# Optimization experiments

Hardware: AMD Instinct MI355X
Metric: run time of the kernel (lower is better)

## Reference

```python
import jax, jax.numpy as jnp
import numpy as np

TEMPERATURE = 0.5


def setup_inputs() -> dict:
    key = jax.random.key(0)
    ks = jax.random.split(key, 12)
    B, N, T = 128, 64, 256
    IN, H, OUT = N + T, 256, 128
    E = N * (N - 1) // 2  # 2016 upper-tri edges per graph
    total_edges = B * E
    inp = {
        "x_topology": jax.random.normal(ks[0], (B, N, N), jnp.float32),
        "x_temporal": jax.random.normal(ks[1], (B, N, T), jnp.float32),
        "gumbel_u": jax.random.uniform(ks[2], (total_edges,), jnp.float32, 1e-6, 1.0),
        # GNNLayer linear
        "W_gnn": jax.random.normal(ks[3], (IN, H), jnp.float32) / np.sqrt(IN),
        "b_gnn": jnp.zeros((H,), jnp.float32),
        # edge heads (input dim 2*H)
        "W_mean": jax.random.normal(ks[4], (2 * H, OUT), jnp.float32) / np.sqrt(2 * H),
        "b_mean": jnp.zeros((OUT,), jnp.float32),
        "W_var": jax.random.normal(ks[5], (2 * H, OUT), jnp.float32) / np.sqrt(2 * H),
        "b_var": jnp.zeros((OUT,), jnp.float32),
        "W_w": jax.random.normal(ks[6], (2 * H, 1), jnp.float32) / np.sqrt(2 * H),
        "b_w": jnp.zeros((1,), jnp.float32),
    }
    return inp


def reference(x_topology, x_temporal, gumbel_u, W_gnn, b_gnn,
              W_mean, b_mean, W_var, b_var, W_w, b_w):
    B, N, _ = x_topology.shape
    T = x_temporal.shape[-1]
    # Upper-triangular fully-connected edge index (no self loops), batched with node offsets.
    row, col = jnp.triu_indices(N, k=1)          # [E]
    E = row.shape[0]
    offs = (jnp.arange(B) * N)[:, None]          # [B,1]
    src = (row[None, :] + offs).reshape(-1)       # [B*E]
    dst = (col[None, :] + offs).reshape(-1)       # [B*E]

    # Node features: concat topology + temporal, flatten batch of graphs.
    x = jnp.concatenate([x_topology, x_temporal], axis=-1).reshape(B * N, N + T)

    # Mean aggregation (PyG aggr='mean'): messages x[src] scattered to dst; 0 for isolated nodes.
    msg_sum = jax.ops.segment_sum(x[src], dst, num_segments=B * N)      # [B*N, N+T]
    cnt = jax.ops.segment_sum(jnp.ones_like(src, x.dtype), dst, num_segments=B * N)
    agg = jnp.where(cnt[:, None] > 0, msg_sum / jnp.maximum(cnt, 1.0)[:, None], 0.0)

    h = jax.nn.relu(agg @ W_gnn + b_gnn)          # [B*N, H]

    # Edge MLP heads on gathered [src||dst] embeddings.
    ef = jnp.concatenate([h[src], h[dst]], axis=-1)        # [B*E, 2H]
    mean = ef @ W_mean + b_mean                             # [B*E, OUT]
    variance = jax.nn.softplus(ef @ W_var + b_var) + 1e-6   # [B*E, OUT]
    weight = jax.nn.sigmoid((ef @ W_w + b_w)[:, 0])          # [B*E]

    # Gumbel-softmax over the flattened edge-weight vector (dim=-1 of a 1-D tensor).
    g = -jnp.log(-jnp.log(gumbel_u))
    gumbel_w = jax.nn.softmax((weight + g) / TEMPERATURE, axis=-1)

    # Gaussian similarity per edge, scatter into dense adjacency.
    sim = jnp.exp(-0.5 * jnp.mean(mean ** 2 / (variance + 1e-8), axis=-1))
    edge_w = sim * gumbel_w                                  # [B*E]

    b_idx = jnp.repeat(jnp.arange(B), E)
    adj = jnp.zeros((B, N, N), x.dtype).at[b_idx, jnp.tile(row, B), jnp.tile(col, B)].set(edge_w)
    return adj
```

## Files before the change

kernel.cpp:

```cpp
#include <hip/hip_runtime.h>
#include <hip/hip_bf16.h>
#include <math.h>

#define Bg   128
#define Nn   64
#define Tt   256
#define INF  320
#define Hd   256
#define OUTD 128
#define Ee   2016
#define TOTE (Bg*Ee)
#define SCOLS 576
#define MROWS 8192

typedef __attribute__((ext_vector_type(8))) short bf16x8;
typedef __attribute__((ext_vector_type(4))) float f32x4;

static __device__ __forceinline__ ushort f2bf(float v) {
    __hip_bfloat16 h = __float2bfloat16(v);
    return *(ushort*)&h;
}

#define CVT_N (INF * Hd)
#define PACK_N (Hd * SCOLS)
#define AGG_BLKS (Bg * 5)

__global__ __launch_bounds__(256) void k_agg_prep(
        const float* __restrict__ topo, const float* __restrict__ temp,
        const float* __restrict__ Wg, const float* __restrict__ Wm,
        const float* __restrict__ Wv, const float* __restrict__ Ww,
        const float* __restrict__ bm, const float* __restrict__ bv,
        const float* __restrict__ bw,
        ushort* __restrict__ agg, ushort* __restrict__ WgbS,
        ushort* __restrict__ WcatS, float* __restrict__ ebias,
        unsigned* __restrict__ red) {
    __shared__ float T[64 * 65];
    const int bid = blockIdx.x;
    const int tid = threadIdx.x;

    if (bid < AGG_BLKS) {
        const int b = bid / 5, ft = bid - 5 * (bid / 5);
        const int row = tid >> 2, seg = tid & 3;
        const float* src = (ft == 0) ? (topo + (size_t)(b * Nn + row) * Nn)
                                     : (temp + (size_t)(b * Nn + row) * Tt + (ft - 1) * 64);
        #pragma unroll
        for (int i = 0; i < 4; ++i) {
            float4 v = *(const float4*)(src + seg * 16 + i * 4);
            float* d = &T[row * 65 + seg * 16 + i * 4];
            d[0] = v.x; d[1] = v.y; d[2] = v.z; d[3] = v.w;
        }
        __syncthreads();
        const int w = tid >> 6, lane = tid & 63;
        #pragma unroll
        for (int k = 0; k < 16; ++k) {
            int f = w * 16 + k;
            float x = T[lane * 65 + f];
            float incl = x;
            #pragma unroll
            for (int o = 1; o < 64; o <<= 1) {
                float t = __shfl_up(incl, o);
                if (lane >= o) incl += t;
            }
            float excl = incl - x;
            T[lane * 65 + f] = lane ? excl * __builtin_amdgcn_rcpf((float)lane) : 0.f;
        }
        __syncthreads();
        const int node = tid >> 2, f0 = (tid & 3) * 16;
        ushort tmp[16];
        #pragma unroll
        for (int i = 0; i < 16; ++i) tmp[i] = f2bf(T[node * 65 + f0 + i]);
        ushort* dst = agg + (size_t)(b * Nn + node) * INF + ft * 64 + f0;
        *(uint4*)dst = *(uint4*)tmp;
        *(uint4*)(dst + 8) = *(uint4*)(tmp + 8);
        return;
    }

    int idx = (bid - AGG_BLKS) * 256 + tid;
    if (idx == 0) { red[0] = 0u; red[1] = 0u; }
    if (idx < CVT_N) {
        int j = idx & 7, lane = (idx >> 3) & 63, ns = (idx >> 9) & 3;
        int rem = idx >> 11;
        int kw = rem % 10, t = rem / 10;
        int n = t * 64 + ns * 16 + (lane & 15);
        int k = kw * 32 + (lane >> 4) * 8 + j;
        WgbS[idx] = f2bf(Wg[k * Hd + n]);
        return;
    }
    idx -= CVT_N;
    if (idx < PACK_N) {
        int j = idx & 7, lane = (idx >> 3) & 63, ns = (idx >> 9) & 3;
        int rem = idx >> 11;
        int kw = rem % 8, t = rem / 8;
        int n = t * 64 + ns * 16 + (lane & 15);
        int k = kw * 32 + (lane >> 4) * 8 + j;
        float v = 0.f;
        if (n < 128)       v = Wm[k * 128 + n];
        else if (n < 256)  v = Wm[(256 + k) * 128 + (n - 128)];
        else if (n < 384)  v = Wv[k * 128 + (n - 256)];
        else if (n < 512)  v = Wv[(256 + k) * 128 + (n - 384)];
        else if (n == 512) v = Ww[k];
        else if (n == 513) v = Ww[256 + k];
        WcatS[idx] = f2bf(v);
        return;
    }
    idx -= PACK_N;
    if (idx >= SCOLS) return;
    float e = 0.f;
    if (idx < 128)                    e = bm[idx];
    else if (idx >= 256 && idx < 384) e = bv[idx - 256];
    else if (idx == 512)              e = bw[0];
    ebias[idx] = e;
}

template<int K>
__global__ __launch_bounds__(256) void k_gemm_direct(const ushort* __restrict__ A,
                                                     const ushort* __restrict__ Bsw,
                                                     const float* __restrict__ bias,
                                                     ushort* __restrict__ Cb,
                                                     float* __restrict__ Cf,
                                                     int N, int relu, int transC) {
    const int tid = threadIdx.x;
    const int w = tid >> 6, lane = tid & 63;
    const int quad = lane >> 4, r16 = lane & 15;
    const int m0 = blockIdx.y * 64, n0 = blockIdx.x * 64;
    const ushort* arow = A + (size_t)(m0 + w * 16 + r16) * K + quad * 8;
    const ushort* bbase = Bsw + (size_t)blockIdx.x * (K / 32) * 2048 + lane * 8;
    f32x4 acc[4] = {};

    #pragma unroll 2
    for (int kw = 0; kw < K / 32; ++kw) {
        bf16x8 af = *(const bf16x8*)(arow + kw * 32);
        const ushort* bp = bbase + kw * 2048;
        bf16x8 b0 = *(const bf16x8*)(bp);
        bf16x8 b1 = *(const bf16x8*)(bp + 512);
        bf16x8 b2 = *(const bf16x8*)(bp + 1024);
        bf16x8 b3 = *(const bf16x8*)(bp + 1536);
        acc[0] = __builtin_amdgcn_mfma_f32_16x16x32_bf16(af, b0, acc[0], 0, 0, 0);
        acc[1] = __builtin_amdgcn_mfma_f32_16x16x32_bf16(af, b1, acc[1], 0, 0, 0);
        acc[2] = __builtin_amdgcn_mfma_f32_16x16x32_bf16(af, b2, acc[2], 0, 0, 0);
        acc[3] = __builtin_amdgcn_mfma_f32_16x16x32_bf16(af, b3, acc[3], 0, 0, 0);
    }

    const int row0 = m0 + w * 16 + quad * 4;
    #pragma unroll
    for (int ns = 0; ns < 4; ++ns) {
        f32x4 a = acc[ns];
        int col = n0 + ns * 16 + r16;
        float bb = bias ? bias[col] : 0.f;
        float vv[4];
        #pragma unroll
        for (int i = 0; i < 4; ++i) {
            float v = a[i] + bb;
            if (relu) v = fmaxf(v, 0.f);
            vv[i] = v;
        }
        if (transC) {
            *(float4*)(Cf + (size_t)col * MROWS + row0) = make_float4(vv[0], vv[1], vv[2], vv[3]);
        } else {
            #pragma unroll
            for (int i = 0; i < 4; ++i) {
                int row2 = row0 + i;
                if (Cb) Cb[(size_t)row2 * N + col] = f2bf(vv[i]);
                else    Cf[(size_t)row2 * N + col] = vv[i];
            }
        }
    }
}

static __device__ __forceinline__ float eterm(float pm, float qm, float pv, float qv) {
    float m = pm + qm;
    float x = pv + qv;
    float sp = fmaxf(x, 0.f) + __logf(1.f + __expf(-fabsf(x)));
    return m * m * __builtin_amdgcn_rcpf(sp + 1.01e-6f);
}

__global__ __launch_bounds__(256) void k_edge4(const float* __restrict__ ST,
                                               const float* __restrict__ gu,
                                               float* __restrict__ numer,
                                               unsigned* __restrict__ red) {
    __shared__ float L[4][16][132];
    __shared__ float sm[256];
    const int p = blockIdx.x % 10, b = blockIdx.x / 10;
    const int G0v[10] = {0,0,0,0,1,1,1,2,2,3};
    const int G1v[10] = {0,1,2,3,1,2,3,2,3,3};
    const int g0 = G0v[p], g1 = G1v[p];
    const int tid = threadIdx.x;

    #pragma unroll
    for (int rep = 0; rep < 8; ++rep) {
        int it = tid + 256 * rep;
        int arr = it >> 9;
        int c = (it >> 2) & 127, nq = it & 3;
        int g = (arr & 1) ? g1 : g0;
        float4 v = *(const float4*)&ST[(size_t)(arr * 128 + c) * MROWS + b * 64 + g * 16 + nq * 4];
        L[arr][nq * 4 + 0][c] = v.x;
        L[arr][nq * 4 + 1][c] = v.y;
        L[arr][nq * 4 + 2][c] = v.z;
        L[arr][nq * 4 + 3][c] = v.w;
    }
    __syncthreads();

    const int i = tid >> 4, j = tid & 15;
    float acc = 0.f;
    #pragma unroll 4
    for (int t = 0; t < 128; t += 4) {
        float4 mi = *(const float4*)&L[0][i][t];
        float4 mj = *(const float4*)&L[1][j][t];
        float4 vi = *(const float4*)&L[2][i][t];
        float4 vj = *(const float4*)&L[3][j][t];
        acc += eterm(mi.x, mj.x, vi.x, vj.x);
        acc += eterm(mi.y, mj.y, vi.y, vj.y);
        acc += eterm(mi.z, mj.z, vi.z, vj.z);
        acc += eterm(mi.w, mj.w, vi.w, vj.w);
    }

    const int ni = g0 * 16 + i, nj = g1 * 16 + j;
    float en = 0.f;
    if (ni < nj) {
        int e = b * Ee + (ni * (127 - ni)) / 2 + (nj - ni - 1);
        float se = __expf(acc * (-1.f / 256.f));
        float wr = ST[(size_t)512 * MROWS + b * 64 + ni]
                 + ST[(size_t)513 * MROWS + b * 64 + nj];
        float w  = __builtin_amdgcn_rcpf(1.f + __expf(-wr));
        float g  = -__logf(-__logf(gu[e]));
        en = __expf((w + g) * 2.0f);
        numer[e] = se * en;
    }
    sm[tid] = en; __syncthreads();
    for (int s = 128; s; s >>= 1) {
        if (tid < s) sm[tid] += sm[tid + s];
        __syncthreads();
    }
    if (!tid) atomicAdd((float*)&red[1], sm[0]);
}

__global__ void k_out(const float* __restrict__ numer, const unsigned* __restrict__ red,
                      float* __restrict__ out) {
    int idx = blockIdx.x * 256 + threadIdx.x;
    if (idx >= Bg * Nn * Nn) return;
    int b = idx >> 12;
    int rem = idx & 4095;
    int r = rem >> 6, c = rem & 63;
    float v = 0.f;
    if (c > r) {
        int e = b * Ee + (r * (127 - r)) / 2 + (c - r - 1);
        float Sinv = __builtin_amdgcn_rcpf(((const float*)red)[1]);
        v = numer[e] * Sinv;
    }
    out[idx] = v;
}

extern "C" void kernel_launch(void* const* d_in, const int* in_sizes, int n_in,
                              void* d_out, int out_size, void* d_ws, size_t ws_size,
                              hipStream_t stream) {
    const float* topo = (const float*)d_in[0];
    const float* temp = (const float*)d_in[1];
    const float* gu   = (const float*)d_in[2];
    const float* Wg   = (const float*)d_in[3];
    const float* bg   = (const float*)d_in[4];
    const float* Wm   = (const float*)d_in[5];
    const float* bm   = (const float*)d_in[6];
    const float* Wv   = (const float*)d_in[7];
    const float* bv   = (const float*)d_in[8];
    const float* Ww   = (const float*)d_in[9];
    const float* bw   = (const float*)d_in[10];
    float* out = (float*)d_out;

    char* ws = (char*)d_ws;
    size_t off = 0;
    auto carve = [&](size_t bytes) { char* p = ws + off; off = (off + bytes + 255) & ~(size_t)255; return p; };

    char*   r1    = carve((size_t)SCOLS * MROWS * 4);
    float*  ST    = (float*)r1;
    ushort* aggb  = (ushort*)r1;
    ushort* hb    = (ushort*)carve((size_t)MROWS * Hd * 2);
    ushort* WgbS  = (ushort*)carve((size_t)CVT_N * 2);
    ushort* WcatS = (ushort*)carve((size_t)PACK_N * 2);
    float*  ebias = (float*)carve((size_t)SCOLS * 4);
    float*  numer = (float*)carve((size_t)TOTE * 4);
    unsigned* red = (unsigned*)carve(256);

    const int prep_blks = (CVT_N + PACK_N + SCOLS + 255) / 256;
    k_agg_prep<<<AGG_BLKS + prep_blks, 256, 0, stream>>>(
        topo, temp, Wg, Wm, Wv, Ww, bm, bv, bw, aggb, WgbS, WcatS, ebias, red);
    k_gemm_direct<INF><<<dim3(Hd / 64, MROWS / 64), 256, 0, stream>>>(
        aggb, WgbS, bg, hb, nullptr, Hd, 1, 0);
    k_gemm_direct<Hd><<<dim3(SCOLS / 64, MROWS / 64), 256, 0, stream>>>(
        hb, WcatS, ebias, nullptr, ST, SCOLS, 0, 1);
    k_edge4<<<Bg * 10, 256, 0, stream>>>(ST, gu, numer, red);
    k_out<<<(Bg * Nn * Nn + 255) / 256, 256, 0, stream>>>(numer, red, out);
}
```

Baseline: 148.1 us.

## Fuse mean-aggregation prefix scan into first GEMM via shared-memory A tile

The mean-aggregation prefix scan now runs inside the first GEMM kernel. Each block builds the bf16 aggregated tile for one graph in LDS and feeds the MFMA loop straight from there, so the intermediate agg buffer is no longer written to and read back from global memory. The second GEMM gets a specialised kernel with a fully unrolled K loop and no runtime branches. In exchange, the scan is recomputed once for each of the 4 output-column blocks per graph, and the larger LDS footprint may lower occupancy.

After: 154.2 us. +4.1%, slower.

```diff
diff --git a/kernel.cpp b/kernel.cpp
--- a/kernel.cpp
+++ b/kernel.cpp
@@ -23,59 +23,13 @@
 
 #define CVT_N (INF * Hd)
 #define PACK_N (Hd * SCOLS)
-#define AGG_BLKS (Bg * 5)
-
-__global__ __launch_bounds__(256) void k_agg_prep(
-        const float* __restrict__ topo, const float* __restrict__ temp,
-        const float* __restrict__ Wg, const float* __restrict__ Wm,
-        const float* __restrict__ Wv, const float* __restrict__ Ww,
-        const float* __restrict__ bm, const float* __restrict__ bv,
-        const float* __restrict__ bw,
-        ushort* __restrict__ agg, ushort* __restrict__ WgbS,
-        ushort* __restrict__ WcatS, float* __restrict__ ebias,
-        unsigned* __restrict__ red) {
-    __shared__ float T[64 * 65];
-    const int bid = blockIdx.x;
-    const int tid = threadIdx.x;
-
-    if (bid < AGG_BLKS) {
-        const int b = bid / 5, ft = bid - 5 * (bid / 5);
-        const int row = tid >> 2, seg = tid & 3;
-        const float* src = (ft == 0) ? (topo + (size_t)(b * Nn + row) * Nn)
-                                     : (temp + (size_t)(b * Nn + row) * Tt + (ft - 1) * 64);
-        #pragma unroll
-        for (int i = 0; i < 4; ++i) {
-            float4 v = *(const float4*)(src + seg * 16 + i * 4);
-            float* d = &T[row * 65 + seg * 16 + i * 4];
-            d[0] = v.x; d[1] = v.y; d[2] = v.z; d[3] = v.w;
-        }
-        __syncthreads();
-        const int w = tid >> 6, lane = tid & 63;
-        #pragma unroll
-        for (int k = 0; k < 16; ++k) {
-            int f = w * 16 + k;
-            float x = T[lane * 65 + f];
-            float incl = x;
-            #pragma unroll
-            for (int o = 1; o < 64; o <<= 1) {
-                float t = __shfl_up(incl, o);
-                if (lane >= o) incl += t;
-            }
-            float excl = incl - x;
-            T[lane * 65 + f] = lane ? excl * __builtin_amdgcn_rcpf((float)lane) : 0.f;
-        }
-        __syncthreads();
-        const int node = tid >> 2, f0 = (tid & 3) * 16;
-        ushort tmp[16];
-        #pragma unroll
-        for (int i = 0; i < 16; ++i) tmp[i] = f2bf(T[node * 65 + f0 + i]);
-        ushort* dst = agg + (size_t)(b * Nn + node) * INF + ft * 64 + f0;
-        *(uint4*)dst = *(uint4*)tmp;
-        *(uint4*)(dst + 8) = *(uint4*)(tmp + 8);
-        return;
-    }
-
-    int idx = (bid - AGG_BLKS) * 256 + tid;
+__global__ void k_prep(const float* __restrict__ Wg, const float* __restrict__ Wm,
+                       const float* __restrict__ Wv, const float* __restrict__ Ww,
+                       const float* __restrict__ bm, const float* __restrict__ bv,
+                       const float* __restrict__ bw,
+                       ushort* __restrict__ WgbS, ushort* __restrict__ WcatS,
+                       float* __restrict__ ebias, unsigned* __restrict__ red) {
+    int idx = blockIdx.x * 256 + threadIdx.x;
     if (idx == 0) { red[0] = 0u; red[1] = 0u; }
     if (idx < CVT_N) {
         int j = idx & 7, lane = (idx >> 3) & 63, ns = (idx >> 9) & 3;
@@ -112,23 +66,98 @@
     ebias[idx] = e;
 }
 
-template<int K>
-__global__ __launch_bounds__(256) void k_gemm_direct(const ushort* __restrict__ A,
-                                                     const ushort* __restrict__ Bsw,
-                                                     const float* __restrict__ bias,
-                                                     ushort* __restrict__ Cb,
-                                                     float* __restrict__ Cf,
-                                                     int N, int relu, int transC) {
+__global__ __launch_bounds__(256) void k_gemm1f(const float* __restrict__ topo,
+                                                const float* __restrict__ temp,
+                                                const ushort* __restrict__ WgbS,
+                                                const float* __restrict__ bias,
+                                                ushort* __restrict__ hb) {
+    __shared__ ushort Abf[64 * 328];
+    __shared__ float T[64 * 65];
+    const int b = blockIdx.y;
+    const int tid = threadIdx.x;
+    const int row = tid >> 2, seg = tid & 3;
+    const int w = tid >> 6, lane = tid & 63;
+    const int quad = lane >> 4, r16 = lane & 15;
+
+    for (int ft = 0; ft < 5; ++ft) {
+        const float* src = (ft == 0) ? (topo + (size_t)(b * Nn + row) * Nn)
+                                     : (temp + (size_t)(b * Nn + row) * Tt + (ft - 1) * 64);
+        #pragma unroll
+        for (int i = 0; i < 4; ++i) {
+            float4 v = *(const float4*)(src + seg * 16 + i * 4);
+            float* d = &T[row * 65 + seg * 16 + i * 4];
+            d[0] = v.x; d[1] = v.y; d[2] = v.z; d[3] = v.w;
+        }
+        __syncthreads();
+        #pragma unroll
+        for (int k = 0; k < 16; ++k) {
+            int f = w * 16 + k;
+            float x = T[lane * 65 + f];
+            float incl = x;
+            #pragma unroll
+            for (int o = 1; o < 64; o <<= 1) {
+                float t = __shfl_up(incl, o);
+                if (lane >= o) incl += t;
+            }
+            float excl = incl - x;
+            T[lane * 65 + f] = lane ? excl * __builtin_amdgcn_rcpf((float)lane) : 0.f;
+        }
+        __syncthreads();
+        {
+            int f0 = seg * 16;
+            ushort tmp[16];
+            #pragma unroll
+            for (int i = 0; i < 16; ++i) tmp[i] = f2bf(T[row * 65 + f0 + i]);
+            *(uint4*)&Abf[row * 328 + ft * 64 + f0]     = *(uint4*)tmp;
+            *(uint4*)&Abf[row * 328 + ft * 64 + f0 + 8] = *(uint4*)(tmp + 8);
+        }
+        __syncthreads();
+    }
+
+    const ushort* bbase = WgbS + (size_t)blockIdx.x * 10 * 2048 + lane * 8;
+    f32x4 acc[4] = {};
+    #pragma unroll
+    for (int kw = 0; kw < 10; ++kw) {
+        bf16x8 af = *(const bf16x8*)&Abf[(w * 16 + r16) * 328 + kw * 32 + quad * 8];
+        const ushort* bp = bbase + kw * 2048;
+        bf16x8 b0 = *(const bf16x8*)(bp);
+        bf16x8 b1 = *(const bf16x8*)(bp + 512);
+        bf16x8 b2 = *(const bf16x8*)(bp + 1024);
+        bf16x8 b3 = *(const bf16x8*)(bp + 1536);
+        acc[0] = __builtin_amdgcn_mfma_f32_16x16x32_bf16(af, b0, acc[0], 0, 0, 0);
+        acc[1] = __builtin_amdgcn_mfma_f32_16x16x32_bf16(af, b1, acc[1], 0, 0, 0);
+        acc[2] = __builtin_amdgcn_mfma_f32_16x16x32_bf16(af, b2, acc[2], 0, 0, 0);
+        acc[3] = __builtin_amdgcn_mfma_f32_16x16x32_bf16(af, b3, acc[3], 0, 0, 0);
+    }
+
+    const int row0 = b * 64 + w * 16 + quad * 4;
+    #pragma unroll
+    for (int ns = 0; ns < 4; ++ns) {
+        f32x4 a = acc[ns];
+        int col = blockIdx.x * 64 + ns * 16 + r16;
+        float bb = bias[col];
+        #pragma unroll
+        for (int i = 0; i < 4; ++i) {
+            float v = fmaxf(a[i] + bb, 0.f);
+            hb[(size_t)(row0 + i) * Hd + col] = f2bf(v);
+        }
+    }
+}
+
+__global__ __launch_bounds__(256) void k_gemm2(const ushort* __restrict__ A,
+                                               const ushort* __restrict__ Bsw,
+                                               const float* __restrict__ bias,
+                                               float* __restrict__ Cf) {
     const int tid = threadIdx.x;
     const int w = tid >> 6, lane = tid & 63;
     const int quad = lane >> 4, r16 = lane & 15;
     const int m0 = blockIdx.y * 64, n0 = blockIdx.x * 64;
-    const ushort* arow = A + (size_t)(m0 + w * 16 + r16) * K + quad * 8;
-    const ushort* bbase = Bsw + (size_t)blockIdx.x * (K / 32) * 2048 + lane * 8;
+    const ushort* arow = A + (size_t)(m0 + w * 16 + r16) * Hd + quad * 8;
+    const ushort* bbase = Bsw + (size_t)blockIdx.x * 8 * 2048 + lane * 8;
     f32x4 acc[4] = {};
 
-    #pragma unroll 2
-    for (int kw = 0; kw < K / 32; ++kw) {
+    #pragma unroll
+    for (int kw = 0; kw < 8; ++kw) {
         bf16x8 af = *(const bf16x8*)(arow + kw * 32);
         const ushort* bp = bbase + kw * 2048;
         bf16x8 b0 = *(const bf16x8*)(bp);
@@ -146,24 +175,9 @@
     for (int ns = 0; ns < 4; ++ns) {
         f32x4 a = acc[ns];
         int col = n0 + ns * 16 + r16;
-        float bb = bias ? bias[col] : 0.f;
-        float vv[4];
-        #pragma unroll
-        for (int i = 0; i < 4; ++i) {
-            float v = a[i] + bb;
-            if (relu) v = fmaxf(v, 0.f);
-            vv[i] = v;
-        }
-        if (transC) {
-            *(float4*)(Cf + (size_t)col * MROWS + row0) = make_float4(vv[0], vv[1], vv[2], vv[3]);
-        } else {
-            #pragma unroll
-            for (int i = 0; i < 4; ++i) {
-                int row2 = row0 + i;
-                if (Cb) Cb[(size_t)row2 * N + col] = f2bf(vv[i]);
-                else    Cf[(size_t)row2 * N + col] = vv[i];
-            }
-        }
+        float bb = bias[col];
+        *(float4*)(Cf + (size_t)col * MROWS + row0) =
+            make_float4(a[0] + bb, a[1] + bb, a[2] + bb, a[3] + bb);
     }
 }
 
@@ -270,9 +284,7 @@
     size_t off = 0;
     auto carve = [&](size_t bytes) { char* p = ws + off; off = (off + bytes + 255) & ~(size_t)255; return p; };
 
-    char*   r1    = carve((size_t)SCOLS * MROWS * 4);
-    float*  ST    = (float*)r1;
-    ushort* aggb  = (ushort*)r1;
+    float*  ST    = (float*)carve((size_t)SCOLS * MROWS * 4);
     ushort* hb    = (ushort*)carve((size_t)MROWS * Hd * 2);
     ushort* WgbS  = (ushort*)carve((size_t)CVT_N * 2);
     ushort* WcatS = (ushort*)carve((size_t)PACK_N * 2);
@@ -280,13 +292,10 @@
     float*  numer = (float*)carve((size_t)TOTE * 4);
     unsigned* red = (unsigned*)carve(256);
 
-    const int prep_blks = (CVT_N + PACK_N + SCOLS + 255) / 256;
-    k_agg_prep<<<AGG_BLKS + prep_blks, 256, 0, stream>>>(
-        topo, temp, Wg, Wm, Wv, Ww, bm, bv, bw, aggb, WgbS, WcatS, ebias, red);
-    k_gemm_direct<INF><<<dim3(Hd / 64, MROWS / 64), 256, 0, stream>>>(
-        aggb, WgbS, bg, hb, nullptr, Hd, 1, 0);
-    k_gemm_direct<Hd><<<dim3(SCOLS / 64, MROWS / 64), 256, 0, stream>>>(
-        hb, WcatS, ebias, nullptr, ST, SCOLS, 0, 1);
+    k_prep<<<(CVT_N + PACK_N + SCOLS + 255) / 256, 256, 0, stream>>>(
+        Wg, Wm, Wv, Ww, bm, bv, bw, WgbS, WcatS, ebias, red);
+    k_gemm1f<<<dim3(Hd / 64, Bg), 256, 0, stream>>>(topo, temp, WgbS, bg, hb);
+    k_gemm2<<<dim3(SCOLS / 64, MROWS / 64), 256, 0, stream>>>(hb, WcatS, ebias, ST);
     k_edge4<<<Bg * 10, 256, 0, stream>>>(ST, gu, numer, red);
     k_out<<<(Bg * Nn * Nn + 255) / 256, 256, 0, stream>>>(numer, red, out);
 }
```
